# Kernel optimization log

Measured on AMD Instinct MI355X. Metric: run time of the kernel, lower is better.

Reference implementation:

```python
import jax, jax.numpy as jnp
import numpy as np

B, T, D = 2, 2048, 2048
N, K, H = 16, 8, 128  # heads, kv heads, head_dim
F = 8192              # ffn hidden


def _apply_rope(x, positions, max_wavelength=10000):
    # x: [B, L, heads, H]; positions: [B, L]
    half = x.shape[-1] // 2
    freq_exponents = (2.0 / x.shape[-1]) * jnp.arange(half, dtype=jnp.float32)
    timescale = max_wavelength ** freq_exponents
    radians = positions.astype(jnp.float32)[..., None] / timescale[None, None, :]
    radians = radians[..., None, :]  # [B, L, 1, half]
    sin, cos = jnp.sin(radians), jnp.cos(radians)
    x1, x2 = jnp.split(x, 2, axis=-1)
    return jnp.concatenate([x1 * cos - x2 * sin, x2 * cos + x1 * sin], axis=-1)


def _rms_norm(x, scale):
    var = jnp.mean(jnp.square(x), axis=-1, keepdims=True)
    return x * jax.lax.rsqrt(var + 1e-6) * (1 + scale)


def setup_inputs() -> dict:
    key = jax.random.key(0)
    ks = jax.random.split(key, 8)
    s = 0.02
    x = jax.random.normal(ks[0], (B, T, D), jnp.float32)
    positions = jnp.broadcast_to(jnp.arange(T, dtype=jnp.int32)[None, :], (B, T))
    causal = jnp.tril(jnp.ones((T, T), dtype=bool))
    attn_mask = jnp.broadcast_to(causal[None, None, :, :], (B, 1, T, T))
    return {
        "x": x,
        "positions": positions,
        "attn_mask": attn_mask,
        "w_q": jax.random.normal(ks[1], (N, D, H), jnp.float32) * s,
        "w_kv": jax.random.normal(ks[2], (2, K, D, H), jnp.float32) * s,
        "w_attn_vec": jax.random.normal(ks[3], (N, H, D), jnp.float32) * s,
        "scale_pre_attn": jax.random.normal(ks[4], (D,), jnp.float32) * s,
        "scale_pre_ffw": jax.random.normal(ks[5], (D,), jnp.float32) * s,
        "w_gating": jax.random.normal(ks[6], (2, D, F), jnp.float32) * s,
        "w_linear": jax.random.normal(ks[7], (F, D), jnp.float32) * s,
    }


def reference(x, positions, attn_mask, w_q, w_kv, w_attn_vec,
              scale_pre_attn, scale_pre_ffw, w_gating, w_linear):
    # pre-attention RMSNorm
    xn = _rms_norm(x, scale_pre_attn)

    # GQA projections
    q = jnp.einsum('BTD,NDH->BTNH', xn, w_q)
    kv = jnp.einsum('BSD,eKDH->eBSKH', xn, w_kv)
    k, v = kv[0], kv[1]

    q = _apply_rope(q, positions) * (H ** -0.5)
    k = _apply_rope(k, positions)

    G = N // K
    q = q.reshape(q.shape[0], q.shape[1], K, G, H)  # B T K G H
    logits = jnp.einsum('BTKGH,BSKH->BKGTS', q, k).astype(jnp.float32)
    big_neg = -2.3819763e38
    masked = jnp.where(attn_mask[:, :, None, :, :], logits, big_neg)
    probs = jax.nn.softmax(masked, axis=-1).astype(k.dtype)
    enc = jnp.einsum('BKGTS,BSKH->BTKGH', probs, v)
    enc = enc.reshape(enc.shape[0], enc.shape[1], N, H)
    attn_out = jnp.einsum('BTNH,NHD->BTD', enc, w_attn_vec)

    # residual + pre-FFN RMSNorm + GeGLU FFN
    residual = x + attn_out
    h = _rms_norm(residual, scale_pre_ffw)
    gate = jax.nn.gelu(jnp.dot(h, w_gating[0]))
    act = gate * jnp.dot(h, w_gating[1])
    out = residual + jnp.dot(act, w_linear)
    return out
```

## Files before the change

### kernel.cpp

```cpp
#include <hip/hip_runtime.h>
#include <hip/hip_bf16.h>


typedef __attribute__((ext_vector_type(8))) short bf16x8;
typedef __attribute__((ext_vector_type(4))) float f32x4;

#define GLP(p) ((const __attribute__((address_space(1))) void*)(p))
#define LDSP(p) ((__attribute__((address_space(3))) void*)(p))

__device__ __forceinline__ float bf2f(unsigned short h) {
  union { unsigned int u; float f; } v; v.u = ((unsigned int)h) << 16; return v.f;
}
__device__ __forceinline__ unsigned short f2bf(float f) {
  union { float f; unsigned int u; } v; v.f = f;
  unsigned int r = v.u + 0x7fffu + ((v.u >> 16) & 1u);
  return (unsigned short)(r >> 16);
}
__device__ __forceinline__ float gelu_f(float x) {
  float t = tanhf(0.7978845608028654f * (x + 0.044715f * x * x * x));
  return 0.5f * x * (1.f + t);
}

template <int IN_F32>
__global__ __launch_bounds__(256) void rmsnorm_kernel(const void* __restrict__ x_,
                                                      const float* __restrict__ scale,
                                                      unsigned short* __restrict__ out) {
  int row = blockIdx.x, tid = threadIdx.x;
  float f[8]; float ss = 0.f;
  if (IN_F32) {
    const float* xr = (const float*)x_ + (size_t)row * 2048 + tid * 8;
#pragma unroll
    for (int i = 0; i < 8; ++i) { f[i] = xr[i]; ss += f[i] * f[i]; }
  } else {
    const unsigned short* xr = (const unsigned short*)x_ + (size_t)row * 2048;
    bf16x8 xv = *(const bf16x8*)(xr + tid * 8);
#pragma unroll
    for (int i = 0; i < 8; ++i) { f[i] = bf2f((unsigned short)xv[i]); ss += f[i] * f[i]; }
  }
#pragma unroll
  for (int off = 32; off >= 1; off >>= 1) ss += __shfl_xor(ss, off);
  __shared__ float red[4];
  if ((tid & 63) == 0) red[tid >> 6] = ss;
  __syncthreads();
  ss = red[0] + red[1] + red[2] + red[3];
  float r = rsqrtf(ss * (1.f / 2048.f) + 1e-6f);
  const float* sv = scale + tid * 8;
  bf16x8 o;
#pragma unroll
  for (int i = 0; i < 8; ++i) o[i] = (short)f2bf(f[i] * r * (1.f + sv[i]));
  *(bf16x8*)(out + (size_t)row * 2048 + tid * 8) = o;
}

__global__ __launch_bounds__(256) void transpose_cast_kernel(const float* __restrict__ in,
                                                             unsigned short* __restrict__ out,
                                                             int R, int ldi, long ibs, long obs) {
  __shared__ float tile[32][33];
  int z = blockIdx.z;
  const float* ip = in + (size_t)z * ibs;
  unsigned short* op = out + (size_t)z * obs;
  int c0 = blockIdx.x * 32, r0 = blockIdx.y * 32;
  int tx = threadIdx.x, ty = threadIdx.y;
#pragma unroll
  for (int i = 0; i < 32; i += 8)
    tile[ty + i][tx] = ip[(size_t)(r0 + ty + i) * ldi + (c0 + tx)];
  __syncthreads();
#pragma unroll
  for (int i = 0; i < 32; i += 8)
    op[(size_t)(c0 + ty + i) * R + (r0 + tx)] = f2bf(tile[tx][ty + i]);
}

__global__ __launch_bounds__(256) void vtrans_kernel(const unsigned short* __restrict__ qkv,
                                                     unsigned short* __restrict__ vT) {
  __shared__ unsigned short tile[32][33];
  int z = blockIdx.z, bb = z >> 3, kh = z & 7;
  int s0 = blockIdx.x * 32, h0 = blockIdx.y * 32;
  int tx = threadIdx.x, ty = threadIdx.y;
  const unsigned short* ip = qkv + ((size_t)bb * 2048) * 4096 + 3072 + kh * 128;
  unsigned short* op = vT + (size_t)z * 128 * 2048;
#pragma unroll
  for (int i = 0; i < 32; i += 8)
    tile[ty + i][tx] = ip[(size_t)(s0 + ty + i) * 4096 + h0 + tx];
  __syncthreads();
#pragma unroll
  for (int i = 0; i < 32; i += 8)
    op[(size_t)(h0 + ty + i) * 2048 + s0 + tx] = tile[tx][ty + i];
}

template <int MODE, int OUT_F32, int ADD_F32>
__global__ __launch_bounds__(256, 2) void gemm_bt(const unsigned short* __restrict__ A, int lda,
                                                  const unsigned short* __restrict__ BT, int Kd,
                                                  int Ncols, void* __restrict__ out_,
                                                  const void* __restrict__ add_) {
  __shared__ unsigned short sA0[128 * 32], sA1[128 * 32];
  __shared__ unsigned short sB0[128 * 32], sB1[128 * 32];
  int tid = threadIdx.x;
  int lane = tid & 63, wave = tid >> 6;
  int quad = lane >> 4, l16 = lane & 15;
  int wr = (wave >> 1) * 64, wc = (wave & 1) * 64;
  long rowBase = (long)blockIdx.y * 128, colBase = (long)blockIdx.x * 128;
  f32x4 acc[4][4];
#pragma unroll
  for (int i = 0; i < 4; ++i)
#pragma unroll
    for (int j = 0; j < 4; ++j) acc[i][j] = (f32x4){0.f, 0.f, 0.f, 0.f};

  const unsigned short* Ag = A + (rowBase + (tid >> 2)) * (size_t)lda + (tid & 3) * 8;
  const unsigned short* Bg = BT + (colBase + (tid >> 2)) * (size_t)Kd + (tid & 3) * 8;
  int wofs = wave * 512;

  __builtin_amdgcn_global_load_lds(GLP(Ag), LDSP(sA0 + wofs), 16, 0, 0);
  __builtin_amdgcn_global_load_lds(GLP(Ag + (size_t)64 * lda), LDSP(sA0 + 2048 + wofs), 16, 0, 0);
  __builtin_amdgcn_global_load_lds(GLP(Bg), LDSP(sB0 + wofs), 16, 0, 0);
  __builtin_amdgcn_global_load_lds(GLP(Bg + (size_t)64 * Kd), LDSP(sB0 + 2048 + wofs), 16, 0, 0);
  Ag += 32; Bg += 32;

  unsigned short *curA = sA0, *nxtA = sA1, *curB = sB0, *nxtB = sB1;
  int nIter = Kd >> 5;
  for (int k = 0; k < nIter; ++k) {
    __syncthreads();
    if (k + 1 < nIter) {
      __builtin_amdgcn_global_load_lds(GLP(Ag), LDSP(nxtA + wofs), 16, 0, 0);
      __builtin_amdgcn_global_load_lds(GLP(Ag + (size_t)64 * lda), LDSP(nxtA + 2048 + wofs), 16, 0, 0);
      __builtin_amdgcn_global_load_lds(GLP(Bg), LDSP(nxtB + wofs), 16, 0, 0);
      __builtin_amdgcn_global_load_lds(GLP(Bg + (size_t)64 * Kd), LDSP(nxtB + 2048 + wofs), 16, 0, 0);
      Ag += 32; Bg += 32;
    }
    bf16x8 af[4], bfr[4];
#pragma unroll
    for (int i = 0; i < 4; ++i) af[i] = *(const bf16x8*)(curA + (wr + i * 16 + l16) * 32 + quad * 8);
#pragma unroll
    for (int j = 0; j < 4; ++j) bfr[j] = *(const bf16x8*)(curB + (wc + j * 16 + l16) * 32 + quad * 8);
#pragma unroll
    for (int i = 0; i < 4; ++i)
#pragma unroll
      for (int j = 0; j < 4; ++j)
        acc[i][j] = __builtin_amdgcn_mfma_f32_16x16x32_bf16(af[i], bfr[j], acc[i][j], 0, 0, 0);
    unsigned short* t;
    t = curA; curA = nxtA; nxtA = t;
    t = curB; curB = nxtB; nxtB = t;
  }
  float* outf = (float*)out_;
  unsigned short* outb = (unsigned short*)out_;
  const float* addf = (const float*)add_;
  const unsigned short* addb = (const unsigned short*)add_;
#pragma unroll
  for (int i = 0; i < 4; ++i)
#pragma unroll
    for (int j = 0; j < 4; ++j)
#pragma unroll
      for (int r = 0; r < 4; ++r) {
        long row = rowBase + wr + i * 16 + quad * 4 + r;
        long col = colBase + wc + j * 16 + l16;
        long idx = row * (long)Ncols + col;
        float v = acc[i][j][r];
        if (MODE == 1) v += (ADD_F32 ? addf[idx] : bf2f(addb[idx]));
        if (OUT_F32) outf[idx] = v; else outb[idx] = f2bf(v);
      }
}

__global__ __launch_bounds__(256, 2) void gemm_gating(const unsigned short* __restrict__ A,
                                                      const unsigned short* __restrict__ BgT,
                                                      const unsigned short* __restrict__ BuT,
                                                      unsigned short* __restrict__ act,
                                                      long colOfs) {
  __shared__ unsigned short sA0[128 * 32], sA1[128 * 32];
  __shared__ unsigned short sG0[128 * 32], sG1[128 * 32];
  __shared__ unsigned short sU0[128 * 32], sU1[128 * 32];
  int tid = threadIdx.x;
  int lane = tid & 63, wave = tid >> 6;
  int quad = lane >> 4, l16 = lane & 15;
  int wr = (wave >> 1) * 64, wc = (wave & 1) * 64;
  long rowBase = (long)blockIdx.y * 128, colBase = (long)blockIdx.x * 128;
  f32x4 gacc[4][4], uacc[4][4];
#pragma unroll
  for (int i = 0; i < 4; ++i)
#pragma unroll
    for (int j = 0; j < 4; ++j) {
      gacc[i][j] = (f32x4){0.f, 0.f, 0.f, 0.f};
      uacc[i][j] = (f32x4){0.f, 0.f, 0.f, 0.f};
    }

  const unsigned short* Ag  = A + (rowBase + (tid >> 2)) * (size_t)2048 + (tid & 3) * 8;
  const unsigned short* Bgg = BgT + (colBase + (tid >> 2)) * (size_t)2048 + (tid & 3) * 8;
  const unsigned short* Bug = BuT + (colBase + (tid >> 2)) * (size_t)2048 + (tid & 3) * 8;
  int wofs = wave * 512;

  __builtin_amdgcn_global_load_lds(GLP(Ag), LDSP(sA0 + wofs), 16, 0, 0);
  __builtin_amdgcn_global_load_lds(GLP(Ag + (size_t)64 * 2048), LDSP(sA0 + 2048 + wofs), 16, 0, 0);
  __builtin_amdgcn_global_load_lds(GLP(Bgg), LDSP(sG0 + wofs), 16, 0, 0);
  __builtin_amdgcn_global_load_lds(GLP(Bgg + (size_t)64 * 2048), LDSP(sG0 + 2048 + wofs), 16, 0, 0);
  __builtin_amdgcn_global_load_lds(GLP(Bug), LDSP(sU0 + wofs), 16, 0, 0);
  __builtin_amdgcn_global_load_lds(GLP(Bug + (size_t)64 * 2048), LDSP(sU0 + 2048 + wofs), 16, 0, 0);
  Ag += 32; Bgg += 32; Bug += 32;

  unsigned short *curA = sA0, *nxtA = sA1, *curG = sG0, *nxtG = sG1, *curU = sU0, *nxtU = sU1;
  for (int k = 0; k < 64; ++k) {
    __syncthreads();
    if (k + 1 < 64) {
      __builtin_amdgcn_global_load_lds(GLP(Ag), LDSP(nxtA + wofs), 16, 0, 0);
      __builtin_amdgcn_global_load_lds(GLP(Ag + (size_t)64 * 2048), LDSP(nxtA + 2048 + wofs), 16, 0, 0);
      __builtin_amdgcn_global_load_lds(GLP(Bgg), LDSP(nxtG + wofs), 16, 0, 0);
      __builtin_amdgcn_global_load_lds(GLP(Bgg + (size_t)64 * 2048), LDSP(nxtG + 2048 + wofs), 16, 0, 0);
      __builtin_amdgcn_global_load_lds(GLP(Bug), LDSP(nxtU + wofs), 16, 0, 0);
      __builtin_amdgcn_global_load_lds(GLP(Bug + (size_t)64 * 2048), LDSP(nxtU + 2048 + wofs), 16, 0, 0);
      Ag += 32; Bgg += 32; Bug += 32;
    }
    bf16x8 af[4], bg[4], bu[4];
#pragma unroll
    for (int i = 0; i < 4; ++i) af[i] = *(const bf16x8*)(curA + (wr + i * 16 + l16) * 32 + quad * 8);
#pragma unroll
    for (int j = 0; j < 4; ++j) bg[j] = *(const bf16x8*)(curG + (wc + j * 16 + l16) * 32 + quad * 8);
#pragma unroll
    for (int j = 0; j < 4; ++j) bu[j] = *(const bf16x8*)(curU + (wc + j * 16 + l16) * 32 + quad * 8);
#pragma unroll
    for (int i = 0; i < 4; ++i)
#pragma unroll
      for (int j = 0; j < 4; ++j) {
        gacc[i][j] = __builtin_amdgcn_mfma_f32_16x16x32_bf16(af[i], bg[j], gacc[i][j], 0, 0, 0);
        uacc[i][j] = __builtin_amdgcn_mfma_f32_16x16x32_bf16(af[i], bu[j], uacc[i][j], 0, 0, 0);
      }
    unsigned short* t;
    t = curA; curA = nxtA; nxtA = t;
    t = curG; curG = nxtG; nxtG = t;
    t = curU; curU = nxtU; nxtU = t;
  }
#pragma unroll
  for (int i = 0; i < 4; ++i)
#pragma unroll
    for (int j = 0; j < 4; ++j)
#pragma unroll
      for (int r = 0; r < 4; ++r) {
        long row = rowBase + wr + i * 16 + quad * 4 + r;
        long col = colBase + wc + j * 16 + l16;
        act[row * 8192 + colOfs + col] = f2bf(gelu_f(gacc[i][j][r]) * uacc[i][j][r]);
      }
}

__global__ __launch_bounds__(256) void rope_kernel(unsigned short* __restrict__ qkv,
                                                   const int* __restrict__ pos) {
  int gid = blockIdx.x * 256 + threadIdx.x;
  int hp = gid & 63;
  int rh = gid >> 6;
  int row = rh / 24;
  int head = rh - row * 24;
  float p = (float)pos[row];
  long cb; float sc;
  if (head < 16) { cb = (long)head * 128; sc = 0.08838834764831845f; }
  else { cb = 2048 + (long)(head - 16) * 128; sc = 1.f; }
  unsigned short* ptr = qkv + (long)row * 4096 + cb;
  float inv = exp2f(-(float)hp * (13.287712379549449f / 64.f));
  float ang = p * inv;
  float s = sinf(ang), c = cosf(ang);
  float x1 = bf2f(ptr[hp]), x2 = bf2f(ptr[hp + 64]);
  ptr[hp]      = f2bf((x1 * c - x2 * s) * sc);
  ptr[hp + 64] = f2bf((x2 * c + x1 * s) * sc);
}

__global__ __launch_bounds__(256, 2) void attn_kernel(const unsigned short* __restrict__ qkv,
                                                      const unsigned short* __restrict__ vT,
                                                      unsigned short* __restrict__ enc) {
  extern __shared__ char smem[];
  unsigned short* sK = (unsigned short*)smem;
  unsigned short* sVT = sK + 64 * 128;
  float* sS = (float*)(smem + 32768);
  unsigned short* sP = (unsigned short*)(smem + 32768 + 16896);
  float* sM = (float*)(smem + 32768 + 16896 + 9216);
  float* sL = sM + 64;
  float* sAl = sL + 64;

  int qt = blockIdx.x, n = blockIdx.y, b = blockIdx.z;
  int tid = threadIdx.x, lane = tid & 63, w = tid >> 6;
  int quad = lane >> 4, l16 = lane & 15;
  int kh = n >> 1;
  long rowQ = (long)b * 2048 + (long)qt * 64;

  bf16x8 qf[4];
  {
    const unsigned short* qp = qkv + (rowQ + w * 16 + l16) * 4096 + n * 128 + quad * 8;
#pragma unroll
    for (int ks = 0; ks < 4; ++ks) qf[ks] = *(const bf16x8*)(qp + ks * 32);
  }
  if (tid < 64) { sM[tid] = -1e30f; sL[tid] = 0.f; }
  f32x4 oacc[8];
#pragma unroll
  for (int t = 0; t < 8; ++t) oacc[t] = (f32x4){0.f, 0.f, 0.f, 0.f};

  int srow = tid >> 2, cg = tid & 3;

  for (int st = 0; st <= qt; ++st) {
    __syncthreads();
#pragma unroll
    for (int it = 0; it < 4; ++it) {
      int idx = it * 256 + tid;
      int r = idx >> 4, c = idx & 15;
      bf16x8 kv8 = *(const bf16x8*)(qkv + ((long)b * 2048 + st * 64 + r) * 4096 + 2048 + kh * 128 + c * 8);
      *(bf16x8*)(sK + r * 128 + ((c ^ (r & 7)) * 8)) = kv8;
    }
#pragma unroll
    for (int it = 0; it < 4; ++it) {
      int idx = it * 256 + tid;
      int h = idx >> 3, c = idx & 7;
      bf16x8 vv8 = *(const bf16x8*)(vT + ((long)(b * 8 + kh) * 128 + h) * 2048 + st * 64 + c * 8);
      *(bf16x8*)(sVT + h * 64 + ((c ^ (h & 7)) * 8)) = vv8;
    }
    __syncthreads();

    f32x4 sacc[4];
#pragma unroll
    for (int nt = 0; nt < 4; ++nt) sacc[nt] = (f32x4){0.f, 0.f, 0.f, 0.f};
#pragma unroll
    for (int ks = 0; ks < 4; ++ks)
#pragma unroll
      for (int nt = 0; nt < 4; ++nt) {
        int r = nt * 16 + l16;
        bf16x8 kf = *(const bf16x8*)(sK + r * 128 + (((ks * 4 + quad) ^ (r & 7)) * 8));
        sacc[nt] = __builtin_amdgcn_mfma_f32_16x16x32_bf16(qf[ks], kf, sacc[nt], 0, 0, 0);
      }
#pragma unroll
    for (int nt = 0; nt < 4; ++nt)
#pragma unroll
      for (int r = 0; r < 4; ++r)
        sS[(w * 16 + quad * 4 + r) * 66 + nt * 16 + l16] = sacc[nt][r];
    __syncthreads();

    float vals[16];
    int tglob = qt * 64 + srow;
    float mx = -1e30f;
#pragma unroll
    for (int j = 0; j < 16; ++j) {
      int col = cg * 16 + j;
      float v = sS[srow * 66 + col];
      if (st * 64 + col > tglob) v = -1e30f;
      vals[j] = v;
      mx = fmaxf(mx, v);
    }
    mx = fmaxf(mx, __shfl_xor(mx, 1));
    mx = fmaxf(mx, __shfl_xor(mx, 2));
    float m_old = sM[srow], l_old = sL[srow];
    float m_new = fmaxf(m_old, mx);
    float alpha = __expf(m_old - m_new);
    float sum = 0.f;
#pragma unroll
    for (int j = 0; j < 16; ++j) { vals[j] = __expf(vals[j] - m_new); sum += vals[j]; }
    sum += __shfl_xor(sum, 1);
    sum += __shfl_xor(sum, 2);
    float l_new = alpha * l_old + sum;
    __syncthreads();

#pragma unroll
    for (int jj = 0; jj < 8; ++jj) {
      unsigned int pk = (unsigned int)f2bf(vals[2 * jj]) | ((unsigned int)f2bf(vals[2 * jj + 1]) << 16);
      *(unsigned int*)(sP + srow * 72 + cg * 16 + jj * 2) = pk;
    }
    if (cg == 0) { sM[srow] = m_new; sL[srow] = l_new; sAl[srow] = alpha; }
    __syncthreads();

#pragma unroll
    for (int r = 0; r < 4; ++r) {
      float al = sAl[w * 16 + quad * 4 + r];
#pragma unroll
      for (int nt = 0; nt < 8; ++nt) oacc[nt][r] *= al;
    }
#pragma unroll
    for (int ks = 0; ks < 2; ++ks) {
      bf16x8 pf = *(const bf16x8*)(sP + (w * 16 + l16) * 72 + ks * 32 + quad * 8);
#pragma unroll
      for (int nt = 0; nt < 8; ++nt) {
        int hh = nt * 16 + l16;
        bf16x8 vf = *(const bf16x8*)(sVT + hh * 64 + (((ks * 4 + quad) ^ (hh & 7)) * 8));
        oacc[nt] = __builtin_amdgcn_mfma_f32_16x16x32_bf16(pf, vf, oacc[nt], 0, 0, 0);
      }
    }
  }

#pragma unroll
  for (int r = 0; r < 4; ++r) {
    float invl = 1.f / sL[w * 16 + quad * 4 + r];
    long trow = rowQ + w * 16 + quad * 4 + r;
#pragma unroll
    for (int nt = 0; nt < 8; ++nt)
      enc[trow * 2048 + n * 128 + nt * 16 + l16] = f2bf(oacc[nt][r] * invl);
  }
}

extern "C" void kernel_launch(void* const* d_in, const int* in_sizes, int n_in,
                              void* d_out, int out_size, void* d_ws, size_t ws_size,
                              hipStream_t stream) {
  const float* x = (const float*)d_in[0];
  const int* positions = (const int*)d_in[1];
  const float* wq = (const float*)d_in[3];
  const float* wkv = (const float*)d_in[4];
  const float* wav = (const float*)d_in[5];
  const float* s_attn = (const float*)d_in[6];
  const float* s_ffw = (const float*)d_in[7];
  const float* wg = (const float*)d_in[8];
  const float* wl = (const float*)d_in[9];
  float* outp = (float*)d_out;

  char* ws = (char*)d_ws;
  size_t o = 0;
  unsigned short* XN = (unsigned short*)(ws + o);    o += (size_t)4096 * 2048 * 2;
  unsigned short* WQKVT = (unsigned short*)(ws + o); o += (size_t)4096 * 2048 * 2;
  unsigned short* WAVT = (unsigned short*)(ws + o);  o += (size_t)2048 * 2048 * 2;
  unsigned short* WGT = (unsigned short*)(ws + o);   o += (size_t)8192 * 2048 * 2;
  unsigned short* QKV = (unsigned short*)(ws + o);   o += (size_t)4096 * 4096 * 2;
  unsigned short* VTb = (unsigned short*)(ws + o);   o += (size_t)16 * 128 * 2048 * 2;
  unsigned short* ACT = (unsigned short*)(ws + o);   o += (size_t)4096 * 8192 * 2;
  unsigned short* ENC = WQKVT;
  unsigned short* RES = QKV;
  unsigned short* HB = XN;

  dim3 b256(256), bT(32, 8);

  rmsnorm_kernel<1><<<4096, b256, 0, stream>>>(x, s_attn, XN);

  transpose_cast_kernel<<<dim3(4, 64, 16), bT, 0, stream>>>(wq, WQKVT, 2048, 128, 262144L, 262144L);
  transpose_cast_kernel<<<dim3(4, 64, 8), bT, 0, stream>>>(wkv, WQKVT + (size_t)2048 * 2048, 2048, 128, 262144L, 262144L);
  transpose_cast_kernel<<<dim3(4, 64, 8), bT, 0, stream>>>(wkv + (size_t)8 * 262144, WQKVT + (size_t)3072 * 2048, 2048, 128, 262144L, 262144L);
  transpose_cast_kernel<<<dim3(64, 64, 1), bT, 0, stream>>>(wav, WAVT, 2048, 2048, 0L, 0L);

  gemm_bt<0, 0, 0><<<dim3(32, 32), b256, 0, stream>>>(XN, 2048, WQKVT, 2048, 4096, QKV, nullptr);

  vtrans_kernel<<<dim3(64, 4, 16), bT, 0, stream>>>(QKV, VTb);

  rope_kernel<<<24576, b256, 0, stream>>>(QKV, positions);

  attn_kernel<<<dim3(32, 16, 2), b256, 59648, stream>>>(QKV, VTb, ENC);

  gemm_bt<1, 0, 1><<<dim3(16, 32), b256, 0, stream>>>(ENC, 2048, WAVT, 2048, 2048, RES, x);

  rmsnorm_kernel<0><<<4096, b256, 0, stream>>>(RES, s_ffw, HB);

  for (int half = 0; half < 2; ++half) {
    long f0 = (long)half * 4096;
    transpose_cast_kernel<<<dim3(128, 64, 1), bT, 0, stream>>>(wg + f0, WGT, 2048, 8192, 0L, 0L);
    transpose_cast_kernel<<<dim3(128, 64, 1), bT, 0, stream>>>(wg + (size_t)2048 * 8192 + f0,
                                                               WGT + (size_t)4096 * 2048, 2048, 8192, 0L, 0L);
    gemm_gating<<<dim3(32, 32), b256, 0, stream>>>(HB, WGT, WGT + (size_t)4096 * 2048, ACT, f0);
  }

  transpose_cast_kernel<<<dim3(64, 256, 1), bT, 0, stream>>>(wl, WGT, 8192, 2048, 0L, 0L);
  gemm_bt<1, 1, 0><<<dim3(16, 32), b256, 0, stream>>>(ACT, 8192, WGT, 8192, 2048, outp, RES);
}
```

Measured before the change: 1.102 ms.

## Replace GEMMs with 8-wave 256-wide tiled kernel using swizzled LDS and staged prefetch

Replaces the 128x128, 4-wave GEMM kernels with one templated 512-thread kernel. It uses 256x256 or 128x256 tiles, a K-step of 64, XOR-swizzled LDS to avoid bank conflicts, and grouped block-ID swizzling for L2 reuse. The main loop is split into four phases with fine-grained barriers, explicit vmcnt waits and s_setprio, so prefetch of the next tile overlaps the MFMA work. The fused gating GEMM is split into two passes: the up projection writes bf16 to ACT, then the gate pass reads it back and applies gelu. This adds an extra round trip of the activation through memory and rounds the up-projection result to bf16 before the multiply.

```diff
diff --git a/kernel.cpp b/kernel.cpp
--- a/kernel.cpp
+++ b/kernel.cpp
@@ -7,6 +7,7 @@
 
 #define GLP(p) ((const __attribute__((address_space(1))) void*)(p))
 #define LDSP(p) ((__attribute__((address_space(3))) void*)(p))
+#define FBAR() do { asm volatile("" ::: "memory"); __builtin_amdgcn_s_barrier(); asm volatile("" ::: "memory"); } while (0)
 
 __device__ __forceinline__ float bf2f(unsigned short h) {
   union { unsigned int u; float f; } v; v.u = ((unsigned int)h) << 16; return v.f;
@@ -86,153 +87,177 @@
     op[(size_t)(h0 + ty + i) * 2048 + s0 + tx] = tile[tx][ty + i];
 }
 
-template <int MODE, int OUT_F32, int ADD_F32>
-__global__ __launch_bounds__(256, 2) void gemm_bt(const unsigned short* __restrict__ A, int lda,
-                                                  const unsigned short* __restrict__ BT, int Kd,
-                                                  int Ncols, void* __restrict__ out_,
-                                                  const void* __restrict__ add_) {
-  __shared__ unsigned short sA0[128 * 32], sA1[128 * 32];
-  __shared__ unsigned short sB0[128 * 32], sB1[128 * 32];
+template <int BM, int MODE, int OUT_F32, int ADD_F32>
+__global__ __launch_bounds__(512, 2) void gemm8p(const unsigned short* __restrict__ A,
+                                                 const unsigned short* __restrict__ BT,
+                                                 int Kd, int ldc, int gx,
+                                                 void* __restrict__ out_,
+                                                 const void* __restrict__ add_) {
+  constexpr int MR = BM / 32;
+  constexpr int MH = MR / 2;
+  constexpr int ASZ = BM * 64;
+  constexpr int BSZ = 256 * 64;
+  __shared__ unsigned short lds[2 * ASZ + 2 * BSZ];
+  unsigned short* aBuf0 = lds;
+  unsigned short* aBuf1 = lds + ASZ;
+  unsigned short* bBuf0 = lds + 2 * ASZ;
+  unsigned short* bBuf1 = lds + 2 * ASZ + BSZ;
+
   int tid = threadIdx.x;
-  int lane = tid & 63, wave = tid >> 6;
+  int lane = tid & 63, w = tid >> 6;
   int quad = lane >> 4, l16 = lane & 15;
-  int wr = (wave >> 1) * 64, wc = (wave & 1) * 64;
-  long rowBase = (long)blockIdx.y * 128, colBase = (long)blockIdx.x * 128;
-  f32x4 acc[4][4];
-#pragma unroll
-  for (int i = 0; i < 4; ++i)
+  int wm = w >> 2, wn = w & 3;
+  int l8 = lane >> 3;
+
+  int nwg = gridDim.x;
+  int id = blockIdx.x;
+  int swzid = (id & 7) * (nwg >> 3) + (id >> 3);
+  int bx = swzid % gx, by = swzid / gx;
+  long rowBase = (long)by * BM, colBase = (long)bx * 256;
+
+  int csw = ((lane & 7) ^ l8) * 8;
+  int rwB = (w >> 2) * 64 + (w & 3) * 8 + l8;
+  int rwA = (BM == 256) ? (w * 8 + l8) : rwB;
+  const unsigned short* aSrc = A + (rowBase + rwA) * (size_t)Kd + csw;
+  const unsigned short* bSrc = BT + (colBase + rwB) * (size_t)Kd + csw;
+
+  auto stgA = [&](unsigned short* dst, int h, int tt) {
+    if (BM == 256) {
+      __builtin_amdgcn_global_load_lds(GLP(aSrc + (size_t)(h * 64) * Kd + (size_t)tt * 64),
+                                       LDSP(dst + (h * 128 + w * 8) * 64), 16, 0, 0);
+      __builtin_amdgcn_global_load_lds(GLP(aSrc + (size_t)(128 + h * 64) * Kd + (size_t)tt * 64),
+                                       LDSP(dst + (h * 128 + 64 + w * 8) * 64), 16, 0, 0);
+    } else {
+      __builtin_amdgcn_global_load_lds(GLP(aSrc + (size_t)(h * 32) * Kd + (size_t)tt * 64),
+                                       LDSP(dst + (h * 64 + w * 8) * 64), 16, 0, 0);
+    }
+  };
+  auto stgB = [&](unsigned short* dst, int h, int tt) {
+    __builtin_amdgcn_global_load_lds(GLP(bSrc + (size_t)(h * 32) * Kd + (size_t)tt * 64),
+                                     LDSP(dst + (h * 128 + w * 8) * 64), 16, 0, 0);
+    __builtin_amdgcn_global_load_lds(GLP(bSrc + (size_t)(128 + h * 32) * Kd + (size_t)tt * 64),
+                                     LDSP(dst + (h * 128 + 64 + w * 8) * 64), 16, 0, 0);
+  };
+
+  int swq0 = (quad * 8) ^ ((l16 & 7) * 8);
+  int swq1 = (32 + quad * 8) ^ ((l16 & 7) * 8);
+  auto rdA = [&](const unsigned short* cur, int i, int kk) -> bf16x8 {
+    int rho = (BM == 256) ? ((i >> 2) * 128 + wm * 64 + (i & 3) * 16 + l16)
+                          : ((i >> 1) * 64 + wm * 32 + (i & 1) * 16 + l16);
+    return *(const bf16x8*)(cur + rho * 64 + (kk ? swq1 : swq0));
+  };
+  auto rdB = [&](const unsigned short* cur, int j, int kk) -> bf16x8 {
+    int rho = (j >> 1) * 128 + wn * 32 + (j & 1) * 16 + l16;
+    return *(const bf16x8*)(cur + rho * 64 + (kk ? swq1 : swq0));
+  };
+
+  f32x4 acc[MR][4];
+#pragma unroll
+  for (int i = 0; i < MR; ++i)
 #pragma unroll
     for (int j = 0; j < 4; ++j) acc[i][j] = (f32x4){0.f, 0.f, 0.f, 0.f};
 
-  const unsigned short* Ag = A + (rowBase + (tid >> 2)) * (size_t)lda + (tid & 3) * 8;
-  const unsigned short* Bg = BT + (colBase + (tid >> 2)) * (size_t)Kd + (tid & 3) * 8;
-  int wofs = wave * 512;
-
-  __builtin_amdgcn_global_load_lds(GLP(Ag), LDSP(sA0 + wofs), 16, 0, 0);
-  __builtin_amdgcn_global_load_lds(GLP(Ag + (size_t)64 * lda), LDSP(sA0 + 2048 + wofs), 16, 0, 0);
-  __builtin_amdgcn_global_load_lds(GLP(Bg), LDSP(sB0 + wofs), 16, 0, 0);
-  __builtin_amdgcn_global_load_lds(GLP(Bg + (size_t)64 * Kd), LDSP(sB0 + 2048 + wofs), 16, 0, 0);
-  Ag += 32; Bg += 32;
-
-  unsigned short *curA = sA0, *nxtA = sA1, *curB = sB0, *nxtB = sB1;
-  int nIter = Kd >> 5;
-  for (int k = 0; k < nIter; ++k) {
-    __syncthreads();
-    if (k + 1 < nIter) {
-      __builtin_amdgcn_global_load_lds(GLP(Ag), LDSP(nxtA + wofs), 16, 0, 0);
-      __builtin_amdgcn_global_load_lds(GLP(Ag + (size_t)64 * lda), LDSP(nxtA + 2048 + wofs), 16, 0, 0);
-      __builtin_amdgcn_global_load_lds(GLP(Bg), LDSP(nxtB + wofs), 16, 0, 0);
-      __builtin_amdgcn_global_load_lds(GLP(Bg + (size_t)64 * Kd), LDSP(nxtB + 2048 + wofs), 16, 0, 0);
-      Ag += 32; Bg += 32;
-    }
-    bf16x8 af[4], bfr[4];
-#pragma unroll
-    for (int i = 0; i < 4; ++i) af[i] = *(const bf16x8*)(curA + (wr + i * 16 + l16) * 32 + quad * 8);
-#pragma unroll
-    for (int j = 0; j < 4; ++j) bfr[j] = *(const bf16x8*)(curB + (wc + j * 16 + l16) * 32 + quad * 8);
-#pragma unroll
-    for (int i = 0; i < 4; ++i)
-#pragma unroll
-      for (int j = 0; j < 4; ++j)
-        acc[i][j] = __builtin_amdgcn_mfma_f32_16x16x32_bf16(af[i], bfr[j], acc[i][j], 0, 0, 0);
-    unsigned short* t;
-    t = curA; curA = nxtA; nxtA = t;
-    t = curB; curB = nxtB; nxtB = t;
-  }
+  stgA(aBuf0, 0, 0); stgB(bBuf0, 0, 0); stgB(bBuf0, 1, 0); stgA(aBuf0, 1, 0);
+  stgA(aBuf1, 0, 1); stgB(bBuf1, 0, 1);
+  if constexpr (BM == 256) asm volatile("s_waitcnt vmcnt(4)" ::: "memory");
+  else                     asm volatile("s_waitcnt vmcnt(3)" ::: "memory");
+  FBAR();
+
+  int NT = Kd >> 6;
+  bf16x8 af[MH][2], bfr0[2][2], bfr1[2][2];
+  for (int t = 0; t < NT; ++t) {
+    unsigned short* aCur = (t & 1) ? aBuf1 : aBuf0;
+    unsigned short* bCur = (t & 1) ? bBuf1 : bBuf0;
+    unsigned short* aNxt = (t & 1) ? aBuf0 : aBuf1;
+    unsigned short* bNxt = (t & 1) ? bBuf0 : bBuf1;
+
+#pragma unroll
+    for (int i = 0; i < MH; ++i) { af[i][0] = rdA(aCur, i, 0); af[i][1] = rdA(aCur, i, 1); }
+#pragma unroll
+    for (int j = 0; j < 2; ++j) { bfr0[j][0] = rdB(bCur, j, 0); bfr0[j][1] = rdB(bCur, j, 1); }
+    if (t + 1 < NT) stgB(bNxt, 1, t + 1);
+    FBAR();
+    __builtin_amdgcn_s_setprio(1);
+#pragma unroll
+    for (int kk = 0; kk < 2; ++kk)
+#pragma unroll
+      for (int i = 0; i < MH; ++i)
+#pragma unroll
+        for (int j = 0; j < 2; ++j)
+          acc[i][j] = __builtin_amdgcn_mfma_f32_16x16x32_bf16(af[i][kk], bfr0[j][kk], acc[i][j], 0, 0, 0);
+    __builtin_amdgcn_s_setprio(0);
+
+#pragma unroll
+    for (int j = 0; j < 2; ++j) { bfr1[j][0] = rdB(bCur, j + 2, 0); bfr1[j][1] = rdB(bCur, j + 2, 1); }
+    if (t + 1 < NT) stgA(aNxt, 1, t + 1);
+    FBAR();
+    __builtin_amdgcn_s_setprio(1);
+#pragma unroll
+    for (int kk = 0; kk < 2; ++kk)
+#pragma unroll
+      for (int i = 0; i < MH; ++i)
+#pragma unroll
+        for (int j = 0; j < 2; ++j)
+          acc[i][j + 2] = __builtin_amdgcn_mfma_f32_16x16x32_bf16(af[i][kk], bfr1[j][kk], acc[i][j + 2], 0, 0, 0);
+    __builtin_amdgcn_s_setprio(0);
+
+#pragma unroll
+    for (int i = 0; i < MH; ++i) { af[i][0] = rdA(aCur, MH + i, 0); af[i][1] = rdA(aCur, MH + i, 1); }
+    if (t + 2 < NT) stgA(aCur, 0, t + 2);
+    FBAR();
+    __builtin_amdgcn_s_setprio(1);
+#pragma unroll
+    for (int kk = 0; kk < 2; ++kk)
+#pragma unroll
+      for (int i = 0; i < MH; ++i)
+#pragma unroll
+        for (int j = 0; j < 2; ++j)
+          acc[MH + i][j] = __builtin_amdgcn_mfma_f32_16x16x32_bf16(af[i][kk], bfr0[j][kk], acc[MH + i][j], 0, 0, 0);
+    __builtin_amdgcn_s_setprio(0);
+
+    if (t + 2 < NT) {
+      stgB(bCur, 0, t + 2);
+      if constexpr (BM == 256) asm volatile("s_waitcnt vmcnt(4)" ::: "memory");
+      else                     asm volatile("s_waitcnt vmcnt(3)" ::: "memory");
+    } else {
+      asm volatile("s_waitcnt vmcnt(0)" ::: "memory");
+    }
+    FBAR();
+    __builtin_amdgcn_s_setprio(1);
+#pragma unroll
+    for (int kk = 0; kk < 2; ++kk)
+#pragma unroll
+      for (int i = 0; i < MH; ++i)
+#pragma unroll
+        for (int j = 0; j < 2; ++j)
+          acc[MH + i][j + 2] = __builtin_amdgcn_mfma_f32_16x16x32_bf16(af[i][kk], bfr1[j][kk], acc[MH + i][j + 2], 0, 0, 0);
+    __builtin_amdgcn_s_setprio(0);
+  }
+
   float* outf = (float*)out_;
   unsigned short* outb = (unsigned short*)out_;
   const float* addf = (const float*)add_;
   const unsigned short* addb = (const unsigned short*)add_;
-#pragma unroll
-  for (int i = 0; i < 4; ++i)
+  long orow = rowBase + wm * (BM / 2);
+  long ocol = colBase + wn * 64 + l16;
+#pragma unroll
+  for (int i = 0; i < MR; ++i)
 #pragma unroll
     for (int j = 0; j < 4; ++j)
 #pragma unroll
-      for (int r = 0; r < 4; ++r) {
-        long row = rowBase + wr + i * 16 + quad * 4 + r;
-        long col = colBase + wc + j * 16 + l16;
-        long idx = row * (long)Ncols + col;
-        float v = acc[i][j][r];
-        if (MODE == 1) v += (ADD_F32 ? addf[idx] : bf2f(addb[idx]));
-        if (OUT_F32) outf[idx] = v; else outb[idx] = f2bf(v);
-      }
-}
-
-__global__ __launch_bounds__(256, 2) void gemm_gating(const unsigned short* __restrict__ A,
-                                                      const unsigned short* __restrict__ BgT,
-                                                      const unsigned short* __restrict__ BuT,
-                                                      unsigned short* __restrict__ act,
-                                                      long colOfs) {
-  __shared__ unsigned short sA0[128 * 32], sA1[128 * 32];
-  __shared__ unsigned short sG0[128 * 32], sG1[128 * 32];
-  __shared__ unsigned short sU0[128 * 32], sU1[128 * 32];
-  int tid = threadIdx.x;
-  int lane = tid & 63, wave = tid >> 6;
-  int quad = lane >> 4, l16 = lane & 15;
-  int wr = (wave >> 1) * 64, wc = (wave & 1) * 64;
-  long rowBase = (long)blockIdx.y * 128, colBase = (long)blockIdx.x * 128;
-  f32x4 gacc[4][4], uacc[4][4];
-#pragma unroll
-  for (int i = 0; i < 4; ++i)
-#pragma unroll
-    for (int j = 0; j < 4; ++j) {
-      gacc[i][j] = (f32x4){0.f, 0.f, 0.f, 0.f};
-      uacc[i][j] = (f32x4){0.f, 0.f, 0.f, 0.f};
-    }
-
-  const unsigned short* Ag  = A + (rowBase + (tid >> 2)) * (size_t)2048 + (tid & 3) * 8;
-  const unsigned short* Bgg = BgT + (colBase + (tid >> 2)) * (size_t)2048 + (tid & 3) * 8;
-  const unsigned short* Bug = BuT + (colBase + (tid >> 2)) * (size_t)2048 + (tid & 3) * 8;
-  int wofs = wave * 512;
-
-  __builtin_amdgcn_global_load_lds(GLP(Ag), LDSP(sA0 + wofs), 16, 0, 0);
-  __builtin_amdgcn_global_load_lds(GLP(Ag + (size_t)64 * 2048), LDSP(sA0 + 2048 + wofs), 16, 0, 0);
-  __builtin_amdgcn_global_load_lds(GLP(Bgg), LDSP(sG0 + wofs), 16, 0, 0);
-  __builtin_amdgcn_global_load_lds(GLP(Bgg + (size_t)64 * 2048), LDSP(sG0 + 2048 + wofs), 16, 0, 0);
-  __builtin_amdgcn_global_load_lds(GLP(Bug), LDSP(sU0 + wofs), 16, 0, 0);
-  __builtin_amdgcn_global_load_lds(GLP(Bug + (size_t)64 * 2048), LDSP(sU0 + 2048 + wofs), 16, 0, 0);
-  Ag += 32; Bgg += 32; Bug += 32;
-
-  unsigned short *curA = sA0, *nxtA = sA1, *curG = sG0, *nxtG = sG1, *curU = sU0, *nxtU = sU1;
-  for (int k = 0; k < 64; ++k) {
-    __syncthreads();
-    if (k + 1 < 64) {
-      __builtin_amdgcn_global_load_lds(GLP(Ag), LDSP(nxtA + wofs), 16, 0, 0);
-      __builtin_amdgcn_global_load_lds(GLP(Ag + (size_t)64 * 2048), LDSP(nxtA + 2048 + wofs), 16, 0, 0);
-      __builtin_amdgcn_global_load_lds(GLP(Bgg), LDSP(nxtG + wofs), 16, 0, 0);
-      __builtin_amdgcn_global_load_lds(GLP(Bgg + (size_t)64 * 2048), LDSP(nxtG + 2048 + wofs), 16, 0, 0);
-      __builtin_amdgcn_global_load_lds(GLP(Bug), LDSP(nxtU + wofs), 16, 0, 0);
-      __builtin_amdgcn_global_load_lds(GLP(Bug + (size_t)64 * 2048), LDSP(nxtU + 2048 + wofs), 16, 0, 0);
-      Ag += 32; Bgg += 32; Bug += 32;
-    }
-    bf16x8 af[4], bg[4], bu[4];
-#pragma unroll
-    for (int i = 0; i < 4; ++i) af[i] = *(const bf16x8*)(curA + (wr + i * 16 + l16) * 32 + quad * 8);
-#pragma unroll
-    for (int j = 0; j < 4; ++j) bg[j] = *(const bf16x8*)(curG + (wc + j * 16 + l16) * 32 + quad * 8);
-#pragma unroll
-    for (int j = 0; j < 4; ++j) bu[j] = *(const bf16x8*)(curU + (wc + j * 16 + l16) * 32 + quad * 8);
-#pragma unroll
-    for (int i = 0; i < 4; ++i)
-#pragma unroll
-      for (int j = 0; j < 4; ++j) {
-        gacc[i][j] = __builtin_amdgcn_mfma_f32_16x16x32_bf16(af[i], bg[j], gacc[i][j], 0, 0, 0);
-        uacc[i][j] = __builtin_amdgcn_mfma_f32_16x16x32_bf16(af[i], bu[j], uacc[i][j], 0, 0, 0);
-      }
-    unsigned short* t;
-    t = curA; curA = nxtA; nxtA = t;
-    t = curG; curG = nxtG; nxtG = t;
-    t = curU; curU = nxtU; nxtU = t;
-  }
-#pragma unroll
-  for (int i = 0; i < 4; ++i)
-#pragma unroll
-    for (int j = 0; j < 4; ++j)
-#pragma unroll
-      for (int r = 0; r < 4; ++r) {
-        long row = rowBase + wr + i * 16 + quad * 4 + r;
-        long col = colBase + wc + j * 16 + l16;
-        act[row * 8192 + colOfs + col] = f2bf(gelu_f(gacc[i][j][r]) * uacc[i][j][r]);
+      for (int rr = 0; rr < 4; ++rr) {
+        long row = orow + i * 16 + quad * 4 + rr;
+        long col = ocol + j * 16;
+        long idx = row * (long)ldc + col;
+        float v = acc[i][j][rr];
+        if (MODE == 0) {
+          outb[idx] = f2bf(v);
+        } else if (MODE == 1) {
+          v += (ADD_F32 ? addf[idx] : bf2f(addb[idx]));
+          if (OUT_F32) outf[idx] = v; else outb[idx] = f2bf(v);
+        } else {
+          outb[idx] = f2bf(gelu_f(v) * bf2f(outb[idx]));
+        }
       }
 }
 
@@ -419,7 +444,7 @@
   transpose_cast_kernel<<<dim3(4, 64, 8), bT, 0, stream>>>(wkv + (size_t)8 * 262144, WQKVT + (size_t)3072 * 2048, 2048, 128, 262144L, 262144L);
   transpose_cast_kernel<<<dim3(64, 64, 1), bT, 0, stream>>>(wav, WAVT, 2048, 2048, 0L, 0L);
 
-  gemm_bt<0, 0, 0><<<dim3(32, 32), b256, 0, stream>>>(XN, 2048, WQKVT, 2048, 4096, QKV, nullptr);
+  gemm8p<256, 0, 0, 0><<<256, 512, 0, stream>>>(XN, WQKVT, 2048, 4096, 16, QKV, nullptr);
 
   vtrans_kernel<<<dim3(64, 4, 16), bT, 0, stream>>>(QKV, VTb);
 
@@ -427,7 +452,7 @@
 
   attn_kernel<<<dim3(32, 16, 2), b256, 59648, stream>>>(QKV, VTb, ENC);
 
-  gemm_bt<1, 0, 1><<<dim3(16, 32), b256, 0, stream>>>(ENC, 2048, WAVT, 2048, 2048, RES, x);
+  gemm8p<128, 1, 0, 1><<<256, 512, 0, stream>>>(ENC, WAVT, 2048, 2048, 8, RES, x);
 
   rmsnorm_kernel<0><<<4096, b256, 0, stream>>>(RES, s_ffw, HB);
 
@@ -436,9 +461,10 @@
     transpose_cast_kernel<<<dim3(128, 64, 1), bT, 0, stream>>>(wg + f0, WGT, 2048, 8192, 0L, 0L);
     transpose_cast_kernel<<<dim3(128, 64, 1), bT, 0, stream>>>(wg + (size_t)2048 * 8192 + f0,
                                                                WGT + (size_t)4096 * 2048, 2048, 8192, 0L, 0L);
-    gemm_gating<<<dim3(32, 32), b256, 0, stream>>>(HB, WGT, WGT + (size_t)4096 * 2048, ACT, f0);
+    gemm8p<256, 0, 0, 0><<<256, 512, 0, stream>>>(HB, WGT + (size_t)4096 * 2048, 2048, 8192, 16, ACT + f0, nullptr);
+    gemm8p<256, 2, 0, 0><<<256, 512, 0, stream>>>(HB, WGT, 2048, 8192, 16, ACT + f0, nullptr);
   }
 
   transpose_cast_kernel<<<dim3(64, 256, 1), bT, 0, stream>>>(wl, WGT, 8192, 2048, 0L, 0L);
-  gemm_bt<1, 1, 0><<<dim3(16, 32), b256, 0, stream>>>(ACT, 8192, WGT, 8192, 2048, outp, RES);
-}
+  gemm8p<128, 1, 1, 0><<<256, 512, 0, stream>>>(ACT, WGT, 8192, 2048, 8, outp, RES);
+}
```

Result: faster. 1.062 ms (-3.6%).
